# Optimization experiments

Measured on AMD Instinct MI355X. Metric: run time of the kernel, lower is better.

## Reference

```python
import jax, jax.numpy as jnp
import numpy as np

N = 50000        # num nodes
E = 1600000      # num edges (avg degree 32)
DIN = 128        # dim_in
DOUT = 256       # dim_out
DA = 32          # dim_atten
SLOPE = 0.2      # leaky_relu negative slope


def setup_inputs() -> dict:
    key = jax.random.key(0)
    ks = jax.random.split(key, 9)
    x = jax.random.normal(ks[0], (N, DIN), dtype=jnp.float32)
    row = jax.random.randint(ks[1], (E,), 0, N, dtype=jnp.int32)
    col = jax.random.randint(ks[2], (E,), 0, N, dtype=jnp.int32)
    adj_val = jax.random.uniform(ks[3], (E,), dtype=jnp.float32)
    # learned params (Linear weights stored as [in, out] for x @ W)
    W_row = (jax.random.normal(ks[4], (DIN, DA)) / np.sqrt(DIN)).astype(jnp.float32)
    W_col = (jax.random.normal(ks[5], (DIN, DA)) / np.sqrt(DIN)).astype(jnp.float32)
    W_x = (jax.random.normal(ks[6], (DIN, DOUT)) / np.sqrt(DIN)).astype(jnp.float32)
    b_x = jnp.zeros((DOUT,), dtype=jnp.float32)
    return {"x": x, "row": row, "col": col, "adj_val": adj_val,
            "W_row": W_row, "W_col": W_col, "W_x": W_x, "b_x": b_x}


def reference(x, row, col, adj_val, W_row, W_col, W_x, b_x):
    # per-node attention projections
    a_row = x @ W_row                      # [N, DA]
    a_col = x @ W_col                      # [N, DA]
    # 'Multiply' attention: per-edge dot product scaled by rsqrt(DA)
    atten = jnp.sum(a_row[row] * a_col[col], axis=1) * jax.lax.rsqrt(jnp.float32(DA))  # [E]
    atten = jnp.where(atten >= 0, atten, SLOPE * atten)   # leaky_relu
    atten = jnp.exp(atten - jnp.max(atten))               # global-max-shifted exp
    # row-sum normalization (segment softmax denominator)
    deg = jax.ops.segment_sum(atten, row, num_segments=N)  # [N]
    atten = atten * (1.0 / (deg + 1e-15))[row]             # [E]
    # atten_combine == 'plus': average with original adjacency values
    vals = (adj_val + atten) * 0.5                         # [E]
    # sparse-dense matmul: out[i] = sum_{e: row[e]==i} vals[e] * x[col[e]]
    out = jax.ops.segment_sum(vals[:, None] * x[col], row, num_segments=N)  # [N, DIN]
    return out @ W_x + b_x                                 # [N, DOUT]
```

## Files before the change

kernel.cpp:

```cpp
#include <hip/hip_runtime.h>


#define DIN   128
#define DOUT  256
#define DA    32
#define SLOPE 0.2f
#define RSQRT_DA 0.17677669529663687f
#define BSH   6
#define BCAP  2560
#define CSTRIDE 32
#define NBMAX 800
#define PB_CHUNK 8192
#define NU    5

typedef unsigned int uint;
typedef unsigned short ushort;
typedef __attribute__((ext_vector_type(8))) short bf16x8;
typedef __attribute__((ext_vector_type(4))) float f32x4;

static __device__ __forceinline__ ushort f2bf(float f) {
  const uint u = __float_as_uint(f);
  return (ushort)((u + 0x7fffu + ((u >> 16) & 1u)) >> 16);
}

__global__ __launch_bounds__(256) void wconv_kernel(
    const float* __restrict__ Wx, ushort* __restrict__ wxt,
    const float* __restrict__ Wr, const float* __restrict__ Wc,
    ushort* __restrict__ wrct, int* __restrict__ bcursor, int nb) {
  __shared__ ushort s[16][DIN];
  const int t = threadIdx.x;
  const int b = blockIdx.x;
  if (b < 16) {
    const int c0 = b * 16;
#pragma unroll
    for (int u = 0; u < 8; ++u) {
      const int k = u * 16 + (t >> 4);
      s[t & 15][k] = f2bf(Wx[(size_t)k * DOUT + c0 + (t & 15)]);
    }
    __syncthreads();
    const int c = t >> 4;
    const int kk = (t & 15) * 8;
    *(uint4*)(wxt + (size_t)(c0 + c) * DIN + kk) = *(const uint4*)&s[c][kk];
  } else if (b < 20) {
    const int c = (b - 16) * 16 + (t >> 4);
    const int k0 = (t & 15) * 8;
    const float* src = (c < DA) ? (Wr + c) : (Wc + (c - DA));
    ushort h[8];
#pragma unroll
    for (int j = 0; j < 8; ++j) h[j] = f2bf(src[(size_t)(k0 + j) * DA]);
    uint4 v;
    v.x = (uint)h[0] | ((uint)h[1] << 16);
    v.y = (uint)h[2] | ((uint)h[3] << 16);
    v.z = (uint)h[4] | ((uint)h[5] << 16);
    v.w = (uint)h[6] | ((uint)h[7] << 16);
    *(uint4*)(wrct + (size_t)c * DIN + k0) = v;
  } else {
    for (int i = t; i < nb; i += 256) bcursor[i * CSTRIDE] = i * BCAP;
  }
}

__global__ __launch_bounds__(512) void super_kernel(
    const float* __restrict__ x, const ushort* __restrict__ wrct,
    float* __restrict__ a_row, ushort* __restrict__ a_colh,
    ushort* __restrict__ xh,
    const int* __restrict__ row, const int* __restrict__ col,
    const float* __restrict__ adj, int* __restrict__ bcursor,
    uint* __restrict__ ibufk, ushort* __restrict__ ibufa,
    int nb, int E, int npart, int n) {
  __shared__ union {
    struct {
      uint   sek[PB_CHUNK];
      ushort sea[PB_CHUNK];
      int hist[NBMAX];
      int lscan[NBMAX];
      int gbase[NBMAX];
    } p;
    ushort xb[32][136];
  } sh;
  const int t = threadIdx.x;

  if ((int)blockIdx.x < npart) {
    int* hist = sh.p.hist;
    int* lscan = sh.p.lscan;
    int* gbase = sh.p.gbase;
    const int e0 = blockIdx.x * PB_CHUNK;
    int myrow[PB_CHUNK / 512];
    for (int b = t; b < nb; b += 512) hist[b] = 0;
    __syncthreads();
#pragma unroll
    for (int u = 0; u < PB_CHUNK / 512; ++u) {
      const int e = e0 + u * 512 + t;
      myrow[u] = (e < E) ? row[e] : -1;
      if (myrow[u] >= 0) atomicAdd(&hist[myrow[u] >> BSH], 1);
    }
    __syncthreads();
    if (t < 64) {
      int running = 0;
      for (int base = 0; base < nb; base += 64) {
        const int idx = base + t;
        const int v = (idx < nb) ? hist[idx] : 0;
        int inc = v;
#pragma unroll
        for (int ofs = 1; ofs < 64; ofs <<= 1) {
          const int o = __shfl_up(inc, ofs, 64);
          if (t >= ofs) inc += o;
        }
        if (idx < nb) lscan[idx] = running + inc - v;
        running += __shfl(inc, 63, 64);
      }
    }
    __syncthreads();
    for (int b = t; b < nb; b += 512) {
      const int c = hist[b];
      gbase[b] = c ? atomicAdd(&bcursor[b * CSTRIDE], c) : 0;
      hist[b] = 0;
    }
    __syncthreads();
#pragma unroll
    for (int u = 0; u < PB_CHUNK / 512; ++u) {
      const int e = e0 + u * 512 + t;
      if (myrow[u] >= 0) {
        const int b = myrow[u] >> BSH;
        const int pos = lscan[b] + atomicAdd(&hist[b], 1);
        sh.p.sek[pos] = ((uint)b << 22) | ((uint)(myrow[u] & 63) << 16) |
                        (uint)col[e];
        sh.p.sea[pos] = f2bf(adj[e]);
      }
    }
    __syncthreads();
    const int cnt_total = min(PB_CHUNK, E - e0);
#pragma unroll
    for (int u = 0; u < PB_CHUNK / 512; ++u) {
      const int el = u * 512 + t;
      if (el < cnt_total) {
        const uint k = sh.p.sek[el];
        const int b = (int)(k >> 22);
        const int gpos = gbase[b] + (el - lscan[b]);
        ibufk[gpos] = k & 0x3fffffu;
        ibufa[gpos] = sh.p.sea[el];
      }
    }
    return;
  }

  const int pb = blockIdx.x - npart;
  const int node0 = pb * 32;
  const float4* xg = (const float4*)(x + (size_t)node0 * DIN);
  if (node0 + 32 <= n) {
#pragma unroll
    for (int u = 0; u < 2; ++u) {
      const int f = t + u * 512;
      const float4 v = xg[f];
      ushort4 h;
      h.x = f2bf(v.x); h.y = f2bf(v.y); h.z = f2bf(v.z); h.w = f2bf(v.w);
      *(ushort4*)&sh.xb[f >> 5][(f & 31) * 4] = h;
      ((ushort4*)(xh + (size_t)node0 * DIN))[f] = h;
    }
  } else {
#pragma unroll
    for (int u = 0; u < 2; ++u) {
      const int f = t + u * 512;
      const int nd = node0 + (f >> 5);
      float4 v;
      if (nd < n) v = xg[f];
      else { v.x = 0.f; v.y = 0.f; v.z = 0.f; v.w = 0.f; }
      ushort4 h;
      h.x = f2bf(v.x); h.y = f2bf(v.y); h.z = f2bf(v.z); h.w = f2bf(v.w);
      *(ushort4*)&sh.xb[f >> 5][(f & 31) * 4] = h;
      if (nd < n) ((ushort4*)(xh + (size_t)node0 * DIN))[f] = h;
    }
  }
  __syncthreads();

  const int w = t >> 6;
  const int l = t & 63;
  const int lr = l & 15;
  const int lk = (l >> 4) * 8;
  const int h2 = w & 1;
  const int q = w >> 1;
  f32x4 acc = {0.f, 0.f, 0.f, 0.f};
#pragma unroll
  for (int kk = 0; kk < 4; ++kk) {
    const bf16x8 a = *(const bf16x8*)&sh.xb[h2 * 16 + lr][kk * 32 + lk];
    const bf16x8 bb =
        *(const bf16x8*)(wrct + (size_t)(q * 16 + lr) * DIN + kk * 32 + lk);
    acc = __builtin_amdgcn_mfma_f32_16x16x32_bf16(a, bb, acc, 0, 0, 0);
  }
  const int colq = q * 16 + lr;
  const int r0 = (l >> 4) * 4;
#pragma unroll
  for (int r = 0; r < 4; ++r) {
    const int node = node0 + h2 * 16 + r0 + r;
    if (node < n) {
      if (colq < DA)
        a_row[(size_t)node * DA + colq] = acc[r] * RSQRT_DA;
      else
        a_colh[(size_t)node * DA + (colq - DA)] = f2bf(acc[r]);
    }
  }
}

#define NODE_BODY(J)                                                    \
  {                                                                     \
    const uint kv = spk[w][half][(J)];                                  \
    const float pv = sp[w][half][(J)];                                  \
    const uint2 xv = xh2[(size_t)(kv & 0xffffu) * 32 + la];             \
    const float av = __uint_as_float(kv & 0xffff0000u);                 \
    const float f0 = __uint_as_float(xv.x << 16);                       \
    const float f1 = __uint_as_float(xv.x & 0xffff0000u);               \
    const float f2 = __uint_as_float(xv.y << 16);                       \
    const float f3 = __uint_as_float(xv.y & 0xffff0000u);               \
    aa0 += av * f0; aa1 += av * f1; aa2 += av * f2; aa3 += av * f3;     \
    ap0 += pv * f0; ap1 += pv * f1; ap2 += pv * f2; ap3 += pv * f3;     \
    deg += pv;                                                          \
  }

__global__ __launch_bounds__(512) void node_kernel(
    const uint* __restrict__ xh, const float* __restrict__ a_row,
    const ushort* __restrict__ a_colh, const int* __restrict__ bcursor,
    const uint* __restrict__ ibufk, const ushort* __restrict__ ibufa,
    ushort* __restrict__ feath, int n) {
  __shared__ uint   eLk[BCAP];
  __shared__ ushort eLa[BCAP];
  __shared__ int    cnt[64];
  __shared__ int    excl[65];
  __shared__ uint   spk[8][2][32];
  __shared__ float  sp[8][2][32];
  __shared__ float  s_ar[8][2][32];
  const int t = threadIdx.x;
  const int b = blockIdx.x;
  const int node0 = b << BSH;
  const int estart = b * BCAP;
  const int ecnt = bcursor[b * CSTRIDE] - estart;

  if (t < 64) cnt[t] = 0;
  __syncthreads();
  uint   myk[NU];
  ushort mya[NU];
#pragma unroll
  for (int u = 0; u < NU; ++u) {
    const int e = u * 512 + t;
    if (e < ecnt) {
      myk[u] = ibufk[estart + e];
      mya[u] = ibufa[estart + e];
      atomicAdd(&cnt[myk[u] >> 16], 1);
    }
  }
  __syncthreads();
  if (t < 64) {
    const int v = cnt[t];
    int inc = v;
#pragma unroll
    for (int ofs = 1; ofs < 64; ofs <<= 1) {
      const int o = __shfl_up(inc, ofs, 64);
      if (t >= ofs) inc += o;
    }
    excl[t] = inc - v;
    if (t == 63) excl[64] = inc;
    cnt[t] = 0;
  }
  __syncthreads();
#pragma unroll
  for (int u = 0; u < NU; ++u) {
    const int e = u * 512 + t;
    if (e < ecnt) {
      const int rl = (int)(myk[u] >> 16);
      const int pos = excl[rl] + atomicAdd(&cnt[rl], 1);
      eLk[pos] = myk[u] & 0xffffu;
      eLa[pos] = mya[u];
    }
  }
  __syncthreads();

  const int w = t >> 6;
  const int lane = t & 63;
  const int half = lane >> 5;
  const int la = lane & 31;
  const uint2* xh2 = (const uint2*)xh;

  for (int pp = 0; pp < 4; ++pp) {
    const int rl0 = (pp * 8 + w) * 2;
    const int i = node0 + rl0 + half;
    const int o0 = excl[rl0];
    const int o1 = excl[rl0 + 1];
    const int o2 = excl[rl0 + 2];
    const int d0 = o1 - o0, d1 = o2 - o1;
    const int myoff = half ? o1 : o0;
    const int myd = half ? d1 : d0;
    const int dmax = max(d0, d1);
    s_ar[w][half][la] = (i < n) ? a_row[(size_t)i * DA + la] : 0.f;

    float aa0 = 0.f, aa1 = 0.f, aa2 = 0.f, aa3 = 0.f;
    float ap0 = 0.f, ap1 = 0.f, ap2 = 0.f, ap3 = 0.f;
    float deg = 0.f;

    for (int base = 0; base < dmax; base += 32) {
      const int m = myd - base;
      if (la < m) {
        const uint c = eLk[myoff + base + la];
        const uint ah = (uint)eLa[myoff + base + la];
        spk[w][half][la] = (ah << 16) | c;
        const uint4* ac = (const uint4*)(a_colh + (size_t)c * DA);
        const float* ar = s_ar[w][half];
        float dot = 0.f;
#pragma unroll
        for (int k = 0; k < 4; ++k) {
          const uint4 q = ac[k];
          const float* a = ar + k * 8;
          dot += __uint_as_float(q.x << 16) * a[0] +
                 __uint_as_float(q.x & 0xffff0000u) * a[1] +
                 __uint_as_float(q.y << 16) * a[2] +
                 __uint_as_float(q.y & 0xffff0000u) * a[3] +
                 __uint_as_float(q.z << 16) * a[4] +
                 __uint_as_float(q.z & 0xffff0000u) * a[5] +
                 __uint_as_float(q.w << 16) * a[6] +
                 __uint_as_float(q.w & 0xffff0000u) * a[7];
        }
        const float lg = (dot >= 0.f) ? dot : SLOPE * dot;
        sp[w][half][la] = __expf(lg);
      } else {
        spk[w][half][la] = 0u;
        sp[w][half][la] = 0.f;
      }
      const int mmax = min(32, dmax - base);
      int j = 0;
      for (; j + 8 <= mmax; j += 8) {
#pragma unroll
        for (int u = 0; u < 8; ++u) NODE_BODY(j + u)
      }
      for (; j < mmax; ++j) NODE_BODY(j)
    }
    if (i < n) {
      const float inv = 0.5f / (deg + 1e-15f);
      ushort4 h;
      h.x = f2bf(0.5f * aa0 + inv * ap0);
      h.y = f2bf(0.5f * aa1 + inv * ap1);
      h.z = f2bf(0.5f * aa2 + inv * ap2);
      h.w = f2bf(0.5f * aa3 + inv * ap3);
      *(ushort4*)(feath + (size_t)i * DIN + la * 4) = h;
    }
  }
}

__global__ __launch_bounds__(256) void gemm_kernel(
    const ushort* __restrict__ feath, const ushort* __restrict__ wxt,
    const float* __restrict__ bx, float* __restrict__ out) {
  const int t = threadIdx.x;
  const int w = t >> 6;
  const int l = t & 63;
  const int row0 = blockIdx.x * 16;
  const int lr = l & 15;
  const int lk = (l >> 4) * 8;
  const int col0 = w * 64;

  f32x4 acc[4] = {f32x4{0.f, 0.f, 0.f, 0.f}, f32x4{0.f, 0.f, 0.f, 0.f},
                  f32x4{0.f, 0.f, 0.f, 0.f}, f32x4{0.f, 0.f, 0.f, 0.f}};
  const ushort* Abase = feath + (size_t)(row0 + lr) * DIN + lk;
#pragma unroll
  for (int kk = 0; kk < 4; ++kk) {
    const bf16x8 a = *(const bf16x8*)(Abase + kk * 32);
#pragma unroll
    for (int ct = 0; ct < 4; ++ct) {
      const bf16x8 b =
          *(const bf16x8*)(wxt + (size_t)(col0 + ct * 16 + lr) * DIN + kk * 32 + lk);
      acc[ct] = __builtin_amdgcn_mfma_f32_16x16x32_bf16(a, b, acc[ct], 0, 0, 0);
    }
  }
  const int crow0 = row0 + (l >> 4) * 4;
#pragma unroll
  for (int ct = 0; ct < 4; ++ct) {
    const int c = col0 + ct * 16 + lr;
    const float bv = bx[c];
#pragma unroll
    for (int r = 0; r < 4; ++r)
      out[(size_t)(crow0 + r) * DOUT + c] = acc[ct][r] + bv;
  }
}

extern "C" void kernel_launch(void* const* d_in, const int* in_sizes, int n_in,
                              void* d_out, int out_size, void* d_ws, size_t ws_size,
                              hipStream_t stream) {
  const float* x   = (const float*)d_in[0];
  const int*   row = (const int*)d_in[1];
  const int*   col = (const int*)d_in[2];
  const float* adj = (const float*)d_in[3];
  const float* Wr  = (const float*)d_in[4];
  const float* Wc  = (const float*)d_in[5];
  const float* Wx  = (const float*)d_in[6];
  const float* bx  = (const float*)d_in[7];
  float* out = (float*)d_out;

  const int n = in_sizes[0] / DIN;
  const int E = in_sizes[1];
  const int nb = (n + 63) >> BSH;
  const int npart = (E + PB_CHUNK - 1) / PB_CHUNK;
  const int nproj = (n + 31) / 32;

  int* w4 = (int*)d_ws;
  float* a_row   = (float*)w4;  w4 += (size_t)n * DA;
  ushort* feath  = (ushort*)w4; w4 += (size_t)n * DIN / 2;
  ushort* a_colh = (ushort*)w4; w4 += (size_t)n * DA / 2;
  uint*   xh     = (uint*)w4;   w4 += (size_t)n * DIN / 2;
  uint*   ibufk  = (uint*)w4;   w4 += (size_t)nb * BCAP;
  ushort* ibufa  = (ushort*)w4; w4 += (size_t)nb * BCAP / 2;
  int*    bcursor= w4;          w4 += (size_t)nb * CSTRIDE;
  ushort* wxt    = (ushort*)w4; w4 += (size_t)DOUT * DIN / 2;
  ushort* wrct   = (ushort*)w4;

  wconv_kernel<<<21, 256, 0, stream>>>(Wx, wxt, Wr, Wc, wrct, bcursor, nb);
  super_kernel<<<npart + nproj, 512, 0, stream>>>(
      x, wrct, a_row, a_colh, (ushort*)xh, row, col, adj, bcursor,
      ibufk, ibufa, nb, E, npart, n);
  node_kernel<<<nb, 512, 0, stream>>>(
      (const uint*)xh, a_row, a_colh, bcursor, ibufk, ibufa, feath, n);
  gemm_kernel<<<n / 16, 256, 0, stream>>>(feath, wxt, bx, out);
}
```

Measured before the change: 249.3 us.

## Fold weight conversion into super kernel and replace cursor init with memset

```diff
diff --git a/kernel.cpp b/kernel.cpp
--- a/kernel.cpp
+++ b/kernel.cpp
@@ -23,50 +23,15 @@
   return (ushort)((u + 0x7fffu + ((u >> 16) & 1u)) >> 16);
 }
 
-__global__ __launch_bounds__(256) void wconv_kernel(
-    const float* __restrict__ Wx, ushort* __restrict__ wxt,
-    const float* __restrict__ Wr, const float* __restrict__ Wc,
-    ushort* __restrict__ wrct, int* __restrict__ bcursor, int nb) {
-  __shared__ ushort s[16][DIN];
-  const int t = threadIdx.x;
-  const int b = blockIdx.x;
-  if (b < 16) {
-    const int c0 = b * 16;
-#pragma unroll
-    for (int u = 0; u < 8; ++u) {
-      const int k = u * 16 + (t >> 4);
-      s[t & 15][k] = f2bf(Wx[(size_t)k * DOUT + c0 + (t & 15)]);
-    }
-    __syncthreads();
-    const int c = t >> 4;
-    const int kk = (t & 15) * 8;
-    *(uint4*)(wxt + (size_t)(c0 + c) * DIN + kk) = *(const uint4*)&s[c][kk];
-  } else if (b < 20) {
-    const int c = (b - 16) * 16 + (t >> 4);
-    const int k0 = (t & 15) * 8;
-    const float* src = (c < DA) ? (Wr + c) : (Wc + (c - DA));
-    ushort h[8];
-#pragma unroll
-    for (int j = 0; j < 8; ++j) h[j] = f2bf(src[(size_t)(k0 + j) * DA]);
-    uint4 v;
-    v.x = (uint)h[0] | ((uint)h[1] << 16);
-    v.y = (uint)h[2] | ((uint)h[3] << 16);
-    v.z = (uint)h[4] | ((uint)h[5] << 16);
-    v.w = (uint)h[6] | ((uint)h[7] << 16);
-    *(uint4*)(wrct + (size_t)c * DIN + k0) = v;
-  } else {
-    for (int i = t; i < nb; i += 256) bcursor[i * CSTRIDE] = i * BCAP;
-  }
-}
-
 __global__ __launch_bounds__(512) void super_kernel(
-    const float* __restrict__ x, const ushort* __restrict__ wrct,
+    const float* __restrict__ x, const float* __restrict__ Wr,
+    const float* __restrict__ Wc, const float* __restrict__ Wx,
     float* __restrict__ a_row, ushort* __restrict__ a_colh,
-    ushort* __restrict__ xh,
+    ushort* __restrict__ xh, ushort* __restrict__ wxt,
     const int* __restrict__ row, const int* __restrict__ col,
     const float* __restrict__ adj, int* __restrict__ bcursor,
     uint* __restrict__ ibufk, ushort* __restrict__ ibufa,
-    int nb, int E, int npart, int n) {
+    int nb, int E, int npart, int nproj, int n) {
   __shared__ union {
     struct {
       uint   sek[PB_CHUNK];
@@ -75,7 +40,11 @@
       int lscan[NBMAX];
       int gbase[NBMAX];
     } p;
-    ushort xb[32][136];
+    struct {
+      ushort xb[32][136];
+      ushort wrc[64][136];
+    } j;
+    ushort s[16][DIN];
   } sh;
   const int t = threadIdx.x;
 
@@ -112,7 +81,7 @@
     __syncthreads();
     for (int b = t; b < nb; b += 512) {
       const int c = hist[b];
-      gbase[b] = c ? atomicAdd(&bcursor[b * CSTRIDE], c) : 0;
+      gbase[b] = b * BCAP + (c ? atomicAdd(&bcursor[b * CSTRIDE], c) : 0);
       hist[b] = 0;
     }
     __syncthreads();
@@ -143,59 +112,85 @@
     return;
   }
 
-  const int pb = blockIdx.x - npart;
-  const int node0 = pb * 32;
-  const float4* xg = (const float4*)(x + (size_t)node0 * DIN);
-  if (node0 + 32 <= n) {
-#pragma unroll
-    for (int u = 0; u < 2; ++u) {
-      const int f = t + u * 512;
-      const float4 v = xg[f];
-      ushort4 h;
-      h.x = f2bf(v.x); h.y = f2bf(v.y); h.z = f2bf(v.z); h.w = f2bf(v.w);
-      *(ushort4*)&sh.xb[f >> 5][(f & 31) * 4] = h;
-      ((ushort4*)(xh + (size_t)node0 * DIN))[f] = h;
-    }
-  } else {
-#pragma unroll
-    for (int u = 0; u < 2; ++u) {
-      const int f = t + u * 512;
-      const int nd = node0 + (f >> 5);
-      float4 v;
-      if (nd < n) v = xg[f];
-      else { v.x = 0.f; v.y = 0.f; v.z = 0.f; v.w = 0.f; }
-      ushort4 h;
-      h.x = f2bf(v.x); h.y = f2bf(v.y); h.z = f2bf(v.z); h.w = f2bf(v.w);
-      *(ushort4*)&sh.xb[f >> 5][(f & 31) * 4] = h;
-      if (nd < n) ((ushort4*)(xh + (size_t)node0 * DIN))[f] = h;
-    }
-  }
-  __syncthreads();
-
-  const int w = t >> 6;
-  const int l = t & 63;
-  const int lr = l & 15;
-  const int lk = (l >> 4) * 8;
-  const int h2 = w & 1;
-  const int q = w >> 1;
-  f32x4 acc = {0.f, 0.f, 0.f, 0.f};
-#pragma unroll
-  for (int kk = 0; kk < 4; ++kk) {
-    const bf16x8 a = *(const bf16x8*)&sh.xb[h2 * 16 + lr][kk * 32 + lk];
-    const bf16x8 bb =
-        *(const bf16x8*)(wrct + (size_t)(q * 16 + lr) * DIN + kk * 32 + lk);
-    acc = __builtin_amdgcn_mfma_f32_16x16x32_bf16(a, bb, acc, 0, 0, 0);
-  }
-  const int colq = q * 16 + lr;
-  const int r0 = (l >> 4) * 4;
-#pragma unroll
-  for (int r = 0; r < 4; ++r) {
-    const int node = node0 + h2 * 16 + r0 + r;
-    if (node < n) {
-      if (colq < DA)
-        a_row[(size_t)node * DA + colq] = acc[r] * RSQRT_DA;
-      else
-        a_colh[(size_t)node * DA + (colq - DA)] = f2bf(acc[r]);
+  if ((int)blockIdx.x < npart + nproj) {
+    const int pb = blockIdx.x - npart;
+    const int node0 = pb * 32;
+    for (int g = t; g < 64 * DIN; g += 512) {
+      const int c = g >> 7, k = g & 127;
+      const float v = (c < DA) ? Wr[(size_t)k * DA + c]
+                               : Wc[(size_t)k * DA + (c - DA)];
+      sh.j.wrc[c][k] = f2bf(v);
+    }
+    const float4* xg = (const float4*)(x + (size_t)node0 * DIN);
+    if (node0 + 32 <= n) {
+#pragma unroll
+      for (int u = 0; u < 2; ++u) {
+        const int f = t + u * 512;
+        const float4 v = xg[f];
+        ushort4 h;
+        h.x = f2bf(v.x); h.y = f2bf(v.y); h.z = f2bf(v.z); h.w = f2bf(v.w);
+        *(ushort4*)&sh.j.xb[f >> 5][(f & 31) * 4] = h;
+        ((ushort4*)(xh + (size_t)node0 * DIN))[f] = h;
+      }
+    } else {
+#pragma unroll
+      for (int u = 0; u < 2; ++u) {
+        const int f = t + u * 512;
+        const int nd = node0 + (f >> 5);
+        float4 v;
+        if (nd < n) v = xg[f];
+        else { v.x = 0.f; v.y = 0.f; v.z = 0.f; v.w = 0.f; }
+        ushort4 h;
+        h.x = f2bf(v.x); h.y = f2bf(v.y); h.z = f2bf(v.z); h.w = f2bf(v.w);
+        *(ushort4*)&sh.j.xb[f >> 5][(f & 31) * 4] = h;
+        if (nd < n) ((ushort4*)(xh + (size_t)node0 * DIN))[f] = h;
+      }
+    }
+    __syncthreads();
+
+    const int w = t >> 6;
+    const int l = t & 63;
+    const int lr = l & 15;
+    const int lk = (l >> 4) * 8;
+    const int h2 = w & 1;
+    const int q = w >> 1;
+    f32x4 acc = {0.f, 0.f, 0.f, 0.f};
+#pragma unroll
+    for (int kk = 0; kk < 4; ++kk) {
+      const bf16x8 a = *(const bf16x8*)&sh.j.xb[h2 * 16 + lr][kk * 32 + lk];
+      const bf16x8 bb = *(const bf16x8*)&sh.j.wrc[q * 16 + lr][kk * 32 + lk];
+      acc = __builtin_amdgcn_mfma_f32_16x16x32_bf16(a, bb, acc, 0, 0, 0);
+    }
+    const int colq = q * 16 + lr;
+    const int r0 = (l >> 4) * 4;
+#pragma unroll
+    for (int r = 0; r < 4; ++r) {
+      const int node = node0 + h2 * 16 + r0 + r;
+      if (node < n) {
+        if (colq < DA)
+          a_row[(size_t)node * DA + colq] = acc[r] * RSQRT_DA;
+        else
+          a_colh[(size_t)node * DA + (colq - DA)] = f2bf(acc[r]);
+      }
+    }
+    return;
+  }
+
+  {
+    const int b3 = blockIdx.x - npart - nproj;
+    const int c0 = b3 * 16;
+    if (t < 256) {
+#pragma unroll
+      for (int u = 0; u < 8; ++u) {
+        const int k = u * 16 + (t >> 4);
+        sh.s[t & 15][k] = f2bf(Wx[(size_t)k * DOUT + c0 + (t & 15)]);
+      }
+    }
+    __syncthreads();
+    if (t < 256) {
+      const int c = t >> 4;
+      const int kk = (t & 15) * 8;
+      *(uint4*)(wxt + (size_t)(c0 + c) * DIN + kk) = *(const uint4*)&sh.s[c][kk];
     }
   }
 }
@@ -220,8 +215,7 @@
     const ushort* __restrict__ a_colh, const int* __restrict__ bcursor,
     const uint* __restrict__ ibufk, const ushort* __restrict__ ibufa,
     ushort* __restrict__ feath, int n) {
-  __shared__ uint   eLk[BCAP];
-  __shared__ ushort eLa[BCAP];
+  __shared__ uint   eL[BCAP];
   __shared__ int    cnt[64];
   __shared__ int    excl[65];
   __shared__ uint   spk[8][2][32];
@@ -231,7 +225,7 @@
   const int b = blockIdx.x;
   const int node0 = b << BSH;
   const int estart = b * BCAP;
-  const int ecnt = bcursor[b * CSTRIDE] - estart;
+  const int ecnt = bcursor[b * CSTRIDE];
 
   if (t < 64) cnt[t] = 0;
   __syncthreads();
@@ -266,8 +260,7 @@
     if (e < ecnt) {
       const int rl = (int)(myk[u] >> 16);
       const int pos = excl[rl] + atomicAdd(&cnt[rl], 1);
-      eLk[pos] = myk[u] & 0xffffu;
-      eLa[pos] = mya[u];
+      eL[pos] = ((uint)mya[u] << 16) | (myk[u] & 0xffffu);
     }
   }
   __syncthreads();
@@ -297,10 +290,9 @@
     for (int base = 0; base < dmax; base += 32) {
       const int m = myd - base;
       if (la < m) {
-        const uint c = eLk[myoff + base + la];
-        const uint ah = (uint)eLa[myoff + base + la];
-        spk[w][half][la] = (ah << 16) | c;
-        const uint4* ac = (const uint4*)(a_colh + (size_t)c * DA);
+        const uint kv = eL[myoff + base + la];
+        spk[w][half][la] = kv;
+        const uint4* ac = (const uint4*)(a_colh + (size_t)(kv & 0xffffu) * DA);
         const float* ar = s_ar[w][half];
         float dot = 0.f;
 #pragma unroll
@@ -404,13 +396,12 @@
   uint*   ibufk  = (uint*)w4;   w4 += (size_t)nb * BCAP;
   ushort* ibufa  = (ushort*)w4; w4 += (size_t)nb * BCAP / 2;
   int*    bcursor= w4;          w4 += (size_t)nb * CSTRIDE;
-  ushort* wxt    = (ushort*)w4; w4 += (size_t)DOUT * DIN / 2;
-  ushort* wrct   = (ushort*)w4;
-
-  wconv_kernel<<<21, 256, 0, stream>>>(Wx, wxt, Wr, Wc, wrct, bcursor, nb);
-  super_kernel<<<npart + nproj, 512, 0, stream>>>(
-      x, wrct, a_row, a_colh, (ushort*)xh, row, col, adj, bcursor,
-      ibufk, ibufa, nb, E, npart, n);
+  ushort* wxt    = (ushort*)w4;
+
+  hipMemsetAsync(bcursor, 0, (size_t)nb * CSTRIDE * sizeof(int), stream);
+  super_kernel<<<npart + nproj + 16, 512, 0, stream>>>(
+      x, Wr, Wc, Wx, a_row, a_colh, (ushort*)xh, wxt, row, col, adj,
+      bcursor, ibufk, ibufa, nb, E, npart, nproj, n);
   node_kernel<<<nb, 512, 0, stream>>>(
       (const uint*)xh, a_row, a_colh, bcursor, ibufk, ibufa, feath, n);
   gemm_kernel<<<n / 16, 256, 0, stream>>>(feath, wxt, bx, out);
```

New measurement: 256.0 us. 2.7% more time.
